# Kernel optimization log

Measured on AMD Instinct MI355X. Metric: run time of the kernel, lower is better.

Reference implementation:

```python
import jax, jax.numpy as jnp
import numpy as np

ENCODER_STRIDE = 320
TEMPERATURE = 1.0


def setup_inputs() -> dict:
    key = jax.random.key(0)
    k1, k2, k3, k4 = jax.random.split(key, 4)
    B, D, T, K = 8, 512, 4096, 4096
    student_features = jax.random.normal(k1, (B, D, T), dtype=jnp.float32)
    codebook = jax.random.normal(k2, (K, D), dtype=jnp.float32)
    teacher_codes = jax.random.randint(k3, (B, T), 0, K, dtype=jnp.int64)
    lengths = jax.random.randint(k4, (B,), 0, T * ENCODER_STRIDE, dtype=jnp.int64)
    return {
        "student_features": student_features,
        "codebook": codebook,
        "teacher_codes": teacher_codes,
        "lengths": lengths,
    }


def reference(student_features, codebook, teacher_codes, lengths):
    B, D, T = student_features.shape
    # length mask over frames: frame t is valid if its start sample < length
    frame_starts = jnp.arange(T, dtype=jnp.int64) * ENCODER_STRIDE  # [T]
    mask = (frame_starts[None, :] < lengths[:, None]).astype(student_features.dtype)  # [B,T]

    z = jnp.transpose(student_features, (0, 2, 1)).reshape(-1, D)  # [N,D], N=B*T

    # cdist p=2: sqrt(|z|^2 + |c|^2 - 2 z.c)
    z2 = jnp.sum(z * z, axis=1, keepdims=True)            # [N,1]
    c2 = jnp.sum(codebook * codebook, axis=1)[None, :]    # [1,K]
    d2 = z2 + c2 - 2.0 * (z @ codebook.T)                 # [N,K]
    dists = jnp.sqrt(jnp.maximum(d2, 1e-12))

    soft_weights = jax.nn.softmax(-dists / TEMPERATURE, axis=1)  # [N,K]
    soft_recon = soft_weights @ codebook                          # [N,D]

    codes_flat = teacher_codes.reshape(-1)                        # [N]
    target_embeddings = jax.lax.stop_gradient(codebook[codes_flat])  # [N,D]

    diff_sq = jnp.mean((soft_recon - target_embeddings) ** 2, axis=1).reshape(B, T)
    loss = jnp.sum(diff_sq * mask) / (jnp.sum(mask) + 1e-8)
    return loss
```

## Files before the change

### kernel.cpp

```cpp
#include <hip/hip_runtime.h>
#include <hip/hip_bf16.h>


#define BB 8
#define DD 512
#define TT 4096
#define KKK 4096
#define ENC_STRIDE 320
#define KT 32
#define NKT (KKK / KT)
#define NW 8
#define ROWS 128
#define KBROW 2056
#define KBBYTES 4112
#define BUFB (8 * KBBYTES)

#define WS_C2    256
#define WS_RTS   16640
#define WS_CBH   32768
#define WS_PART  4227072ULL
#define WS_ML    (WS_PART + 67108864ULL)
#define WS_NEED  (WS_ML + 524288ULL)

typedef __attribute__((ext_vector_type(8))) short bf16x8;
typedef __attribute__((ext_vector_type(4))) float f32x4;

union FragU { bf16x8 v; uint2 h2[2]; ushort us[8]; unsigned long long q[2]; uint4 u4; };

static __device__ __forceinline__ ushort f2bf(float x) {
  unsigned u = __float_as_uint(x);
  unsigned r = (u + 0x7FFFu + ((u >> 16) & 1u)) >> 16;
  return (ushort)r;
}
static __device__ __forceinline__ uint2 f4tobf(float4 v) {
  uint2 r;
  r.x = (unsigned)f2bf(v.x) | ((unsigned)f2bf(v.y) << 16);
  r.y = (unsigned)f2bf(v.z) | ((unsigned)f2bf(v.w) << 16);
  return r;
}
static __device__ __forceinline__ unsigned pk2bf(float lo, float hi) {
  return (__float_as_uint(lo) >> 16) | (__float_as_uint(hi) & 0xFFFF0000u);
}
static __device__ __forceinline__ float bfh2f(ushort h) {
  return __uint_as_float(((unsigned)h) << 16);
}
static __device__ __forceinline__ float fsqrtf(float x) {
  float r; asm("v_sqrt_f32 %0, %1" : "=v"(r) : "v"(x)); return r;
}
static __device__ __forceinline__ void gld_lds16(const void* g, void* l) {
  __builtin_amdgcn_global_load_lds(
      (const __attribute__((address_space(1))) unsigned*)g,
      (__attribute__((address_space(3))) unsigned*)l, 16, 0, 0);
}
static __device__ __forceinline__ unsigned lds_addr(const void* p) {
  return (unsigned)(size_t)(const __attribute__((address_space(3))) char*)p;
}

__global__ __launch_bounds__(256) void vq_prep(const float* __restrict__ cb,
                                               float* __restrict__ c2,
                                               ushort* __restrict__ cbh) {
  int k = blockIdx.x * 4 + (threadIdx.x >> 6);
  int lane = threadIdx.x & 63;
  const float4* p = (const float4*)(cb + (size_t)k * DD + lane * 8);
  float4 a = p[0], b = p[1];
  if (cbh) {
    uint2 pa = f4tobf(a), pb = f4tobf(b);
    *(uint4*)(cbh + (size_t)k * DD + lane * 8) = make_uint4(pa.x, pa.y, pb.x, pb.y);
  }
  float s = a.x*a.x + a.y*a.y + a.z*a.z + a.w*a.w
          + b.x*b.x + b.y*b.y + b.z*b.z + b.w*b.w;
  #pragma unroll
  for (int m = 1; m <= 32; m <<= 1) s += __shfl_xor(s, m);
  if (lane == 0) c2[k] = s;
}

__global__ void vq_plan(const int* __restrict__ lens, int* __restrict__ hdr,
                        int* __restrict__ rts) {
  int n = 0;
  for (int b2 = 0; b2 < BB; ++b2) {
    int v = (lens[b2] + (ENC_STRIDE - 1)) / ENC_STRIDE;
    v = v < TT ? v : TT;
    int tiles = (v + 127) >> 7;
    for (int t = 0; t < tiles; ++t) rts[n++] = (b2 << 5) | t;
  }
  hdr[0] = n;
  hdr[1] = (n * 128 + 255) >> 8;
  hdr[2] = n * 128;
}

__global__ __launch_bounds__(512, 2) void vq_main_ws(
    const float* __restrict__ sf,
    const ushort* __restrict__ cbh,
    const float* __restrict__ c2,
    const int* __restrict__ hdr,
    const int* __restrict__ rts,
    ushort* __restrict__ recon_p,
    float* __restrict__ ml) {
  __shared__ __align__(128) ushort cs[4][8][KBROW];
  __shared__ __align__(16) ushort wlds[2][NW][16][40];
  __shared__ float  alds[2][ROWS];
  __shared__ float  llds[ROWS];
  __shared__ int    flagv[128];

  const int Q = hdr[1], total = hdr[2];
  int start = blockIdx.x * Q;
  if (Q == 0 || start >= total) return;
  int end = start + Q;
  end = end < total ? end : total;
  int slot = blockIdx.x * 2;

  const int tid = threadIdx.x;
  const int w  = tid >> 6;
  const int l  = tid & 63;
  const int lg = l >> 4;
  const int ln = l & 15;
  const int sbase = (w * 4 + ((l >> 1) & 3)) * DD + (l >> 3) * 16 + (l & 1) * 8;
  const unsigned score_lane = (unsigned)((ln >> 2) * KBBYTES + (ln & 3) * 32
                                         + (lg >> 1) * 128 + (lg & 1) * 16);
  const unsigned tr_lane = (unsigned)(lg * KBBYTES + w * 512 + ln * 8);
  const unsigned cs0a = lds_addr(&cs[0][0][0]);

  while (start < end) {
    const int rt = start >> 7;
    const int k0 = start & 127;
    int seg_end = (rt + 1) << 7;
    seg_end = seg_end < end ? seg_end : end;
    const int klen = seg_end - start;
    const int rtv = rts[rt];
    const int b  = rtv >> 5;
    const int t0 = (rtv & 31) << 7;

    for (int i2 = tid; i2 < klen; i2 += 512) flagv[i2] = 0;

    const float* sfb = sf + (size_t)b * DD * TT;
    const int trow = t0 + w * 16 + ln;
    bf16x8 za[16];
    float z2 = 0.f;
    #pragma unroll
    for (int f = 0; f < 16; ++f) {
      #pragma unroll
      for (int j = 0; j < 8; ++j) {
        int d = f * 32 + lg * 8 + j;
        float v = __builtin_nontemporal_load(&sfb[(size_t)d * TT + trow]);
        z2 += v * v;
        za[f][j] = (short)f2bf(v);
      }
    }
    z2 += __shfl_xor(z2, 16);
    z2 += __shfl_xor(z2, 32);

    auto stage = [&](int kta, int buf) {
      const ushort* gb = cbh + (size_t)kta * KT * DD + sbase;
      ushort* lb = &cs[buf][w][0];
      #pragma unroll
      for (int q = 0; q < 4; ++q) gld_lds16(gb + q * 128, lb + q * 512);
    };

    stage(k0, 0);
    if (klen > 1) stage(k0 + 1, 1);
    if (klen > 2) stage(k0 + 2, 2);

    float mrow = -1e30f, lrow = 0.f;
    f32x4 acc[8][4];
    #pragma unroll
    for (int r = 0; r < 8; ++r)
      #pragma unroll
      for (int nt = 0; nt < 4; ++nt) acc[r][nt] = (f32x4){0.f, 0.f, 0.f, 0.f};

    f32x4 sc0, sc1;
    auto scores = [&](int sbuf) {
      const char* csb = (const char*)&cs[sbuf][0][0];
      f32x4 e0s = (f32x4){0,0,0,0}, o0s = (f32x4){0,0,0,0};
      f32x4 e1s = (f32x4){0,0,0,0}, o1s = (f32x4){0,0,0,0};
      __builtin_amdgcn_s_setprio(1);
      #pragma unroll
      for (int f = 0; f < 8; ++f) {
        bf16x8 ae0 = *(const bf16x8*)(csb + score_lane + (2 * f) * 256);
        bf16x8 ao0 = *(const bf16x8*)(csb + score_lane + (2 * f + 1) * 256);
        bf16x8 ae1 = *(const bf16x8*)(csb + score_lane + 16448 + (2 * f) * 256);
        bf16x8 ao1 = *(const bf16x8*)(csb + score_lane + 16448 + (2 * f + 1) * 256);
        e0s = __builtin_amdgcn_mfma_f32_16x16x32_bf16(ae0, za[2 * f],     e0s, 0, 0, 0);
        o0s = __builtin_amdgcn_mfma_f32_16x16x32_bf16(ao0, za[2 * f + 1], o0s, 0, 0, 0);
        e1s = __builtin_amdgcn_mfma_f32_16x16x32_bf16(ae1, za[2 * f],     e1s, 0, 0, 0);
        o1s = __builtin_amdgcn_mfma_f32_16x16x32_bf16(ao1, za[2 * f + 1], o1s, 0, 0, 0);
      }
      __builtin_amdgcn_s_setprio(0);
      sc0 = e0s + o0s;
      sc1 = e1s + o1s;
    };

    auto softmax_full = [&](int kta, int li) {
      const float4 c2a = *(const float4*)(c2 + kta * KT + lg * 4);
      const float4 c2b = *(const float4*)(c2 + kta * KT + 16 + lg * 4);
      float c2v[8] = {c2a.x, c2a.y, c2a.z, c2a.w, c2b.x, c2b.y, c2b.z, c2b.w};
      float sv[8];
      #pragma unroll
      for (int v = 0; v < 4; ++v) {
        sv[v]     = -fsqrtf(fmaxf(z2 + c2v[v]     - 2.f * sc0[v], 1e-12f));
        sv[4 + v] = -fsqrtf(fmaxf(z2 + c2v[4 + v] - 2.f * sc1[v], 1e-12f));
      }
      float lmax = sv[0];
      #pragma unroll
      for (int i = 1; i < 8; ++i) lmax = fmaxf(lmax, sv[i]);
      float tmax = fmaxf(lmax, __shfl_xor(lmax, 16));
      tmax = fmaxf(tmax, __shfl_xor(tmax, 32));
      float el[8], lsum = 0.f;
      #pragma unroll
      for (int i = 0; i < 8; ++i) { el[i] = __expf(sv[i] - lmax); lsum += el[i]; }
      const bool defer = (li > 0) && (tmax <= mrow + 8.f);
      const float mnew = defer ? mrow : fmaxf(tmax, mrow);
      const float factor = __expf(lmax - mnew);
      float esum = lsum * factor;
      esum += __shfl_xor(esum, 16);
      esum += __shfl_xor(esum, 32);
      const float alpha = (li > 0 && !defer) ? __expf(mrow - mnew) : 1.f;
      lrow = lrow * alpha + esum;
      mrow = mnew;
      uint4 pk;
      pk.x = pk2bf(el[0] * factor, el[1] * factor);
      pk.y = pk2bf(el[2] * factor, el[3] * factor);
      pk.z = pk2bf(el[4] * factor, el[5] * factor);
      pk.w = pk2bf(el[6] * factor, el[7] * factor);
      *(uint4*)&wlds[li & 1][w][ln][lg * 8] = pk;
      if (lg == 0) alds[li & 1][w * 16 + ln] = alpha;
      if (li > 0 && !__all(defer) && l == 0) flagv[li] = 1;
    };

    auto recon_full = [&](int lim1) {
      const int s = lim1 & 1;
      const unsigned trb = cs0a + (unsigned)(lim1 & 3) * BUFB + tr_lane;
      unsigned long long tq0[4], tq1[4];
      #pragma unroll
      for (int nt = 0; nt < 4; ++nt) {
        asm volatile("ds_read_b64_tr_b16 %0, %2 offset:%3\n\t"
                     "ds_read_b64_tr_b16 %1, %2 offset:%4"
                     : "=&v"(tq0[nt]), "=&v"(tq1[nt])
                     : "v"(trb), "i"(nt * 128), "i"(16448 + nt * 128));
      }
      const int flg = flagv[lim1];
      asm volatile("s_waitcnt lgkmcnt(0)" ::: "memory");
      __builtin_amdgcn_sched_barrier(0);
      if (flg) {
        #pragma unroll
        for (int r = 0; r < 8; ++r)
          #pragma unroll
          for (int v = 0; v < 4; ++v) {
            float av = alds[s][r * 16 + lg * 4 + v];
            #pragma unroll
            for (int nt = 0; nt < 4; ++nt) acc[r][nt][v] *= av;
          }
      }
      FragU cf[4];
      #pragma unroll
      for (int nt = 0; nt < 4; ++nt) { cf[nt].q[0] = tq0[nt]; cf[nt].q[1] = tq1[nt]; }
      __builtin_amdgcn_s_setprio(1);
      #pragma unroll
      for (int rh = 0; rh < 2; ++rh) {
        bf16x8 wa4[4];
        #pragma unroll
        for (int r4 = 0; r4 < 4; ++r4)
          wa4[r4] = *(const bf16x8*)&wlds[s][rh * 4 + r4][ln][lg * 8];
        #pragma unroll
        for (int r4 = 0; r4 < 4; ++r4)
          #pragma unroll
          for (int nt = 0; nt < 4; ++nt)
            acc[rh * 4 + r4][nt] = __builtin_amdgcn_mfma_f32_16x16x32_bf16(
                wa4[r4], cf[nt].v, acc[rh * 4 + r4][nt], 0, 0, 0);
      }
      __builtin_amdgcn_s_setprio(0);
    };

    __syncthreads();
    scores(0);
    softmax_full(k0, 0);

    if (w < 4) {
      #pragma unroll 1
      for (int li = 1; li < klen; ++li) {
        __syncthreads();
        if (li + 2 < klen) stage(k0 + li + 2, (li + 2) & 3);
        scores(li & 3);
        softmax_full(k0 + li, li);
        recon_full(li - 1);
      }
    } else {
      #pragma unroll 1
      for (int li = 1; li < klen; ++li) {
        __syncthreads();
        if (li + 2 < klen) stage(k0 + li + 2, (li + 2) & 3);
        recon_full(li - 1);
        scores(li & 3);
        softmax_full(k0 + li, li);
      }
    }

    __syncthreads();
    recon_full(klen - 1);

    if (lg == 0) {
      llds[w * 16 + ln] = lrow;
      float2 mlv; mlv.x = mrow; mlv.y = lrow;
      *(float2*)&ml[(size_t)(slot * 128 + w * 16 + ln) * 2] = mlv;
    }
    __syncthreads();
    {
      ushort* rp = recon_p + (size_t)slot * (128 * 512);
      #pragma unroll
      for (int r = 0; r < 8; ++r) {
        #pragma unroll
        for (int v = 0; v < 4; ++v) {
          const int row = r * 16 + lg * 4 + v;
          const float lv = llds[row];
          #pragma unroll
          for (int nt = 0; nt < 4; ++nt) {
            const int d = w * 64 + nt * 16 + ln;
            rp[row * 512 + d] = f2bf(acc[r][nt][v] / lv);
          }
        }
      }
    }
    __syncthreads();

    start += klen;
    slot++;
  }
}

__global__ __launch_bounds__(512) void vq_merge(
    const ushort* __restrict__ recon_p, const float* __restrict__ ml,
    const int* __restrict__ hdr, const int* __restrict__ rts,
    const int* __restrict__ lens, const float* __restrict__ cb,
    const int* __restrict__ codes, float* __restrict__ num) {
  __shared__ float red[64];
  const int i = blockIdx.x;
  const int nact = hdr[0];
  if (i >= nact) return;
  const int Q = hdr[1], total = hdr[2];
  const int rtv = rts[i];
  const int b = rtv >> 5;
  const int t0 = (rtv & 31) << 7;
  int vcount = (lens[b] + (ENC_STRIDE - 1)) / ENC_STRIDE;
  vcount = vcount < TT ? vcount : TT;

  const int tid = threadIdx.x;
  const int rl = tid >> 3;
  const int q  = tid & 7;
  const int r  = blockIdx.y * 64 + rl;
  const int flat0 = i << 7, flat1 = flat0 + 128;
  int c_lo = flat0 / Q;
  int c_hi = (flat1 - 1) / Q;
  c_hi = c_hi < 255 ? c_hi : 255;

  float M = -1e30f;
  for (int c = c_lo; c <= c_hi; ++c) {
    const int cs_ = c * Q;
    int ce = cs_ + Q; ce = ce < total ? ce : total;
    if (cs_ >= flat1 || ce <= flat0) continue;
    const int slot = c * 2 + (i - (cs_ >> 7));
    M = fmaxf(M, ml[(size_t)(slot * 128 + r) * 2]);
  }
  float L = 0.f;
  for (int c = c_lo; c <= c_hi; ++c) {
    const int cs_ = c * Q;
    int ce = cs_ + Q; ce = ce < total ? ce : total;
    if (cs_ >= flat1 || ce <= flat0) continue;
    const int slot = c * 2 + (i - (cs_ >> 7));
    const float m_ = ml[(size_t)(slot * 128 + r) * 2];
    const float l_ = ml[(size_t)(slot * 128 + r) * 2 + 1];
    L += l_ * __expf(m_ - M);
  }
  const float invL = 1.f / L;

  const int tc = codes[b * TT + t0 + r];
  const float* targ = cb + (size_t)tc * DD;

  float psum = 0.f;
  #pragma unroll 1
  for (int ch = 0; ch < 8; ++ch) {
    const int d0 = q * 64 + ch * 8;
    float rec[8] = {0.f, 0.f, 0.f, 0.f, 0.f, 0.f, 0.f, 0.f};
    for (int c = c_lo; c <= c_hi; ++c) {
      const int cs_ = c * Q;
      int ce = cs_ + Q; ce = ce < total ? ce : total;
      if (cs_ >= flat1 || ce <= flat0) continue;
      const int slot = c * 2 + (i - (cs_ >> 7));
      const float m_ = ml[(size_t)(slot * 128 + r) * 2];
      const float l_ = ml[(size_t)(slot * 128 + r) * 2 + 1];
      const float wn = l_ * __expf(m_ - M) * invL;
      const ushort* rp = recon_p + (size_t)slot * (128 * 512) + r * 512 + d0;
      FragU u; u.u4 = *(const uint4*)rp;
      #pragma unroll
      for (int j = 0; j < 8; ++j) rec[j] += wn * bfh2f(u.us[j]);
    }
    const float4 tg0 = *(const float4*)(targ + d0);
    const float4 tg1 = *(const float4*)(targ + d0 + 4);
    float tg[8] = {tg0.x, tg0.y, tg0.z, tg0.w, tg1.x, tg1.y, tg1.z, tg1.w};
    #pragma unroll
    for (int j = 0; j < 8; ++j) { float df = rec[j] - tg[j]; psum += df * df; }
  }
  psum += __shfl_xor(psum, 1);
  psum += __shfl_xor(psum, 2);
  psum += __shfl_xor(psum, 4);
  if (q == 0) red[rl] = ((t0 + r) < vcount) ? psum * (1.f / DD) : 0.f;
  __syncthreads();
  if (tid < 64) {
    float val = red[tid];
    val += __shfl_xor(val, 1);
    val += __shfl_xor(val, 2);
    val += __shfl_xor(val, 4);
    val += __shfl_xor(val, 8);
    val += __shfl_xor(val, 16);
    val += __shfl_xor(val, 32);
    if (tid == 0) atomicAdd(num, val);
  }
}

template <int GLD>
__global__ __launch_bounds__(512, 2) void vq_main(
    const float* __restrict__ sf, const float* __restrict__ cb,
    const ushort* __restrict__ cbh, const int* __restrict__ codes,
    const int* __restrict__ lens, const float* __restrict__ c2,
    float* __restrict__ num) {
  __shared__ __align__(128) ushort cs[4][8][KBROW];
  __shared__ __align__(16) ushort wlds[2][NW][16][40];
  __shared__ float  alds[2][ROWS];
  __shared__ float  llds[ROWS];
  __shared__ float  diffred[ROWS];
  __shared__ int    flagv[NKT];

  const int bid = blockIdx.x;
  const int b  = bid >> 5;
  const int t0 = (bid & 31) << 7;
  const int len = lens[b];
  int vcount = (len + (ENC_STRIDE - 1)) / ENC_STRIDE;
  vcount = vcount < TT ? vcount : TT;
  if (t0 >= vcount) return;

  const int tid = threadIdx.x;
  const int w  = tid >> 6;
  const int l  = tid & 63;
  const int lg = l >> 4;
  const int ln = l & 15;

  for (int i = tid; i < ROWS; i += 512) diffred[i] = 0.f;
  for (int i = tid; i < NKT; i += 512) flagv[i] = 0;

  const float* sfb = sf + (size_t)b * DD * TT;
  const int trow = t0 + w * 16 + ln;
  bf16x8 za[16];
  float z2 = 0.f;
  #pragma unroll
  for (int f = 0; f < 16; ++f) {
    #pragma unroll
    for (int j = 0; j < 8; ++j) {
      int d = f * 32 + lg * 8 + j;
      float v = __builtin_nontemporal_load(&sfb[(size_t)d * TT + trow]);
      z2 += v * v;
      za[f][j] = (short)f2bf(v);
    }
  }
  z2 += __shfl_xor(z2, 16);
  z2 += __shfl_xor(z2, 32);

  const int sbase = (w * 4 + ((l >> 1) & 3)) * DD + (l >> 3) * 16 + (l & 1) * 8;
  auto stage = [&](int kt, int buf) {
    if (GLD) {
      const ushort* gb = cbh + (size_t)kt * KT * DD + sbase;
      ushort* lb = &cs[buf][w][0];
      #pragma unroll
      for (int q = 0; q < 4; ++q) gld_lds16(gb + q * 128, lb + q * 512);
    } else {
      const float* gb = cb + (size_t)kt * KT * DD + sbase;
      #pragma unroll
      for (int q = 0; q < 4; ++q) {
        float4 v0 = *(const float4*)(gb + q * 128);
        float4 v1 = *(const float4*)(gb + q * 128 + 4);
        uint2 a0 = f4tobf(v0), a1 = f4tobf(v1);
        *(uint4*)&cs[buf][w][q * 512 + l * 8] = make_uint4(a0.x, a0.y, a1.x, a1.y);
      }
    }
  };

  stage(0, 0); stage(1, 1); stage(2, 2);

  float mrow = -1e30f, lrow = 0.f;
  f32x4 acc[8][4];
  #pragma unroll
  for (int r = 0; r < 8; ++r)
    #pragma unroll
    for (int nt = 0; nt < 4; ++nt) acc[r][nt] = (f32x4){0.f, 0.f, 0.f, 0.f};

  const unsigned score_lane = (unsigned)((ln >> 2) * KBBYTES + (ln & 3) * 32
                                         + (lg >> 1) * 128 + (lg & 1) * 16);
  const unsigned tr_lane = (unsigned)(lg * KBBYTES + w * 512 + ln * 8);
  const unsigned cs0a = lds_addr(&cs[0][0][0]);

  f32x4 sc0, sc1;
  auto scores = [&](int sbuf) {
    const char* csb = (const char*)&cs[sbuf][0][0];
    f32x4 e0s = (f32x4){0,0,0,0}, o0s = (f32x4){0,0,0,0};
    f32x4 e1s = (f32x4){0,0,0,0}, o1s = (f32x4){0,0,0,0};
    __builtin_amdgcn_s_setprio(1);
    #pragma unroll
    for (int f = 0; f < 8; ++f) {
      bf16x8 ae0 = *(const bf16x8*)(csb + score_lane + (2 * f) * 256);
      bf16x8 ao0 = *(const bf16x8*)(csb + score_lane + (2 * f + 1) * 256);
      bf16x8 ae1 = *(const bf16x8*)(csb + score_lane + 16448 + (2 * f) * 256);
      bf16x8 ao1 = *(const bf16x8*)(csb + score_lane + 16448 + (2 * f + 1) * 256);
      e0s = __builtin_amdgcn_mfma_f32_16x16x32_bf16(ae0, za[2 * f],     e0s, 0, 0, 0);
      o0s = __builtin_amdgcn_mfma_f32_16x16x32_bf16(ao0, za[2 * f + 1], o0s, 0, 0, 0);
      e1s = __builtin_amdgcn_mfma_f32_16x16x32_bf16(ae1, za[2 * f],     e1s, 0, 0, 0);
      o1s = __builtin_amdgcn_mfma_f32_16x16x32_bf16(ao1, za[2 * f + 1], o1s, 0, 0, 0);
    }
    __builtin_amdgcn_s_setprio(0);
    sc0 = e0s + o0s;
    sc1 = e1s + o1s;
  };

  auto softmax_full = [&](int kta, int li) {
    const float4 c2a = *(const float4*)(c2 + kta * KT + lg * 4);
    const float4 c2b = *(const float4*)(c2 + kta * KT + 16 + lg * 4);
    float c2v[8] = {c2a.x, c2a.y, c2a.z, c2a.w, c2b.x, c2b.y, c2b.z, c2b.w};
    float sv[8];
    #pragma unroll
    for (int v = 0; v < 4; ++v) {
      sv[v]     = -fsqrtf(fmaxf(z2 + c2v[v]     - 2.f * sc0[v], 1e-12f));
      sv[4 + v] = -fsqrtf(fmaxf(z2 + c2v[4 + v] - 2.f * sc1[v], 1e-12f));
    }
    float lmax = sv[0];
    #pragma unroll
    for (int i = 1; i < 8; ++i) lmax = fmaxf(lmax, sv[i]);
    float tmax = fmaxf(lmax, __shfl_xor(lmax, 16));
    tmax = fmaxf(tmax, __shfl_xor(tmax, 32));
    float el[8], lsum = 0.f;
    #pragma unroll
    for (int i = 0; i < 8; ++i) { el[i] = __expf(sv[i] - lmax); lsum += el[i]; }
    const bool defer = (li > 0) && (tmax <= mrow + 8.f);
    const float mnew = defer ? mrow : fmaxf(tmax, mrow);
    const float factor = __expf(lmax - mnew);
    float esum = lsum * factor;
    esum += __shfl_xor(esum, 16);
    esum += __shfl_xor(esum, 32);
    const float alpha = (li > 0 && !defer) ? __expf(mrow - mnew) : 1.f;
    lrow = lrow * alpha + esum;
    mrow = mnew;
    uint4 pk;
    pk.x = pk2bf(el[0] * factor, el[1] * factor);
    pk.y = pk2bf(el[2] * factor, el[3] * factor);
    pk.z = pk2bf(el[4] * factor, el[5] * factor);
    pk.w = pk2bf(el[6] * factor, el[7] * factor);
    *(uint4*)&wlds[li & 1][w][ln][lg * 8] = pk;
    if (lg == 0) alds[li & 1][w * 16 + ln] = alpha;
    if (li > 0 && !__all(defer) && l == 0) flagv[li] = 1;
  };

  auto recon_full = [&](int lim1) {
    const int s = lim1 & 1;
    const unsigned trb = cs0a + (unsigned)(lim1 & 3) * BUFB + tr_lane;
    unsigned long long tq0[4], tq1[4];
    #pragma unroll
    for (int nt = 0; nt < 4; ++nt) {
      asm volatile("ds_read_b64_tr_b16 %0, %2 offset:%3\n\t"
                   "ds_read_b64_tr_b16 %1, %2 offset:%4"
                   : "=&v"(tq0[nt]), "=&v"(tq1[nt])
                   : "v"(trb), "i"(nt * 128), "i"(16448 + nt * 128));
    }
    const int flg = flagv[lim1];
    asm volatile("s_waitcnt lgkmcnt(0)" ::: "memory");
    __builtin_amdgcn_sched_barrier(0);
    if (flg) {
      #pragma unroll
      for (int r = 0; r < 8; ++r)
        #pragma unroll
        for (int v = 0; v < 4; ++v) {
          float av = alds[s][r * 16 + lg * 4 + v];
          #pragma unroll
          for (int nt = 0; nt < 4; ++nt) acc[r][nt][v] *= av;
        }
    }
    FragU cf[4];
    #pragma unroll
    for (int nt = 0; nt < 4; ++nt) { cf[nt].q[0] = tq0[nt]; cf[nt].q[1] = tq1[nt]; }
    __builtin_amdgcn_s_setprio(1);
    #pragma unroll
    for (int rh = 0; rh < 2; ++rh) {
      bf16x8 wa4[4];
      #pragma unroll
      for (int r4 = 0; r4 < 4; ++r4)
        wa4[r4] = *(const bf16x8*)&wlds[s][rh * 4 + r4][ln][lg * 8];
      #pragma unroll
      for (int r4 = 0; r4 < 4; ++r4)
        #pragma unroll
        for (int nt = 0; nt < 4; ++nt)
          acc[rh * 4 + r4][nt] = __builtin_amdgcn_mfma_f32_16x16x32_bf16(
              wa4[r4], cf[nt].v, acc[rh * 4 + r4][nt], 0, 0, 0);
    }
    __builtin_amdgcn_s_setprio(0);
  };

  __syncthreads();
  scores(0);
  softmax_full(0, 0);

  if (w < 4) {
    #pragma unroll 1
    for (int it = 1; it < NKT; ++it) {
      __syncthreads();
      if (it + 2 < NKT) stage(it + 2, (it + 2) & 3);
      scores(it & 3);
      softmax_full(it, it);
      recon_full(it - 1);
    }
  } else {
    #pragma unroll 1
    for (int it = 1; it < NKT; ++it) {
      __syncthreads();
      if (it + 2 < NKT) stage(it + 2, (it + 2) & 3);
      recon_full(it - 1);
      scores(it & 3);
      softmax_full(it, it);
    }
  }

  __syncthreads();
  recon_full(NKT - 1);

  if (lg == 0) llds[w * 16 + ln] = lrow;
  __syncthreads();
  const int* tcodes = codes + b * TT + t0;
  #pragma unroll
  for (int r = 0; r < 8; ++r) {
    float pv[4];
    #pragma unroll
    for (int v = 0; v < 4; ++v) {
      const int row = r * 16 + lg * 4 + v;
      const float lv = llds[row];
      const int tc = tcodes[row];
      const float* erow = cb + (size_t)tc * DD + w * 64;
      float ps = 0.f;
      #pragma unroll
      for (int nt = 0; nt < 4; ++nt) {
        float rc = acc[r][nt][v] / lv;
        float df = rc - erow[nt * 16 + ln];
        ps += df * df;
      }
      pv[v] = ps;
    }
    #pragma unroll
    for (int v = 0; v < 4; ++v) {
      pv[v] += __shfl_xor(pv[v], 1);
      pv[v] += __shfl_xor(pv[v], 2);
      pv[v] += __shfl_xor(pv[v], 4);
      pv[v] += __shfl_xor(pv[v], 8);
    }
    if (ln == 0) {
      #pragma unroll
      for (int v = 0; v < 4; ++v)
        atomicAdd(&diffred[r * 16 + lg * 4 + v], pv[v]);
    }
  }
  __syncthreads();
  if (tid < ROWS) {
    float val = (t0 + tid < vcount) ? diffred[tid] * (1.f / DD) : 0.f;
    val += __shfl_xor(val, 1);
    val += __shfl_xor(val, 2);
    val += __shfl_xor(val, 4);
    val += __shfl_xor(val, 8);
    val += __shfl_xor(val, 16);
    val += __shfl_xor(val, 32);
    if ((tid & 63) == 0) atomicAdd(num, val);
  }
}

__global__ void vq_finalize(const float* __restrict__ num,
                            const int* __restrict__ lens,
                            float* __restrict__ out) {
  float denom = 0.f;
  for (int b = 0; b < BB; ++b) {
    int v = (lens[b] + (ENC_STRIDE - 1)) / ENC_STRIDE;
    v = v < TT ? v : TT;
    denom += (float)v;
  }
  out[0] = num[0] / (denom + 1e-8f);
}

extern "C" void kernel_launch(void* const* d_in, const int* in_sizes, int n_in,
                              void* d_out, int out_size, void* d_ws, size_t ws_size,
                              hipStream_t stream) {
  const float* sf    = (const float*)d_in[0];
  const float* cb    = (const float*)d_in[1];
  const int*   codes = (const int*)d_in[2];
  const int*   lens  = (const int*)d_in[3];
  float* out = (float*)d_out;
  float* num = (float*)d_ws;
  int*   hdr = (int*)((char*)d_ws + 16);
  float* c2  = (float*)((char*)d_ws + WS_C2);
  int*   rts = (int*)((char*)d_ws + WS_RTS);
  const size_t need_gld = WS_CBH + (size_t)KKK * DD * sizeof(ushort);
  ushort* cbh = (ws_size >= need_gld) ? (ushort*)((char*)d_ws + WS_CBH) : nullptr;

  (void)hipMemsetAsync(d_ws, 0, 4, stream);
  vq_prep<<<KKK / 4, 256, 0, stream>>>(cb, c2, cbh);

  if (cbh && ws_size >= WS_NEED) {
    ushort* recon_p = (ushort*)((char*)d_ws + WS_PART);
    float*  mlp     = (float*)((char*)d_ws + WS_ML);
    vq_plan<<<1, 1, 0, stream>>>(lens, hdr, rts);
    vq_main_ws<<<256, 512, 0, stream>>>(sf, cbh, c2, hdr, rts, recon_p, mlp);
    vq_merge<<<dim3(256, 2), 512, 0, stream>>>(recon_p, mlp, hdr, rts, lens, cb, codes, num);
  } else {
    const int grid = (BB * TT) / ROWS;
    if (cbh)
      vq_main<1><<<grid, 512, 0, stream>>>(sf, cb, cbh, codes, lens, c2, num);
    else
      vq_main<0><<<grid, 512, 0, stream>>>(sf, cb, cbh, codes, lens, c2, num);
  }
  vq_finalize<<<1, 1, 0, stream>>>(num, lens, out);
}
```

Before: 375.7 us.

## Fold tile planning into prep kernel and read score operands from global for half the waves

After: 575.8 us. 53.3% more time.

```diff
diff --git a/kernel.cpp b/kernel.cpp
--- a/kernel.cpp
+++ b/kernel.cpp
@@ -58,7 +58,22 @@
 
 __global__ __launch_bounds__(256) void vq_prep(const float* __restrict__ cb,
                                                float* __restrict__ c2,
-                                               ushort* __restrict__ cbh) {
+                                               ushort* __restrict__ cbh,
+                                               const int* __restrict__ lens,
+                                               int* __restrict__ hdr,
+                                               int* __restrict__ rts) {
+  if (blockIdx.x == 0 && threadIdx.x == 0 && hdr) {
+    int n = 0;
+    for (int b2 = 0; b2 < BB; ++b2) {
+      int v = (lens[b2] + (ENC_STRIDE - 1)) / ENC_STRIDE;
+      v = v < TT ? v : TT;
+      int tiles = (v + 127) >> 7;
+      for (int t = 0; t < tiles; ++t) rts[n++] = (b2 << 5) | t;
+    }
+    hdr[0] = n;
+    hdr[1] = (n * 128 + 255) >> 8;
+    hdr[2] = n * 128;
+  }
   int k = blockIdx.x * 4 + (threadIdx.x >> 6);
   int lane = threadIdx.x & 63;
   const float4* p = (const float4*)(cb + (size_t)k * DD + lane * 8);
@@ -72,20 +87,6 @@
   #pragma unroll
   for (int m = 1; m <= 32; m <<= 1) s += __shfl_xor(s, m);
   if (lane == 0) c2[k] = s;
-}
-
-__global__ void vq_plan(const int* __restrict__ lens, int* __restrict__ hdr,
-                        int* __restrict__ rts) {
-  int n = 0;
-  for (int b2 = 0; b2 < BB; ++b2) {
-    int v = (lens[b2] + (ENC_STRIDE - 1)) / ENC_STRIDE;
-    v = v < TT ? v : TT;
-    int tiles = (v + 127) >> 7;
-    for (int t = 0; t < tiles; ++t) rts[n++] = (b2 << 5) | t;
-  }
-  hdr[0] = n;
-  hdr[1] = (n * 128 + 255) >> 8;
-  hdr[2] = n * 128;
 }
 
 __global__ __launch_bounds__(512, 2) void vq_main_ws(
@@ -119,6 +120,8 @@
                                          + (lg >> 1) * 128 + (lg & 1) * 16);
   const unsigned tr_lane = (unsigned)(lg * KBBYTES + w * 512 + ln * 8);
   const unsigned cs0a = lds_addr(&cs[0][0][0]);
+  const ushort* gsc0 = cbh + (size_t)ln * DD + lg * 8;
+  const ushort* gsc1 = cbh + (size_t)(16 + ln) * DD + lg * 8;
 
   while (start < end) {
     const int rt = start >> 7;
@@ -168,23 +171,42 @@
       for (int nt = 0; nt < 4; ++nt) acc[r][nt] = (f32x4){0.f, 0.f, 0.f, 0.f};
 
     f32x4 sc0, sc1;
-    auto scores = [&](int sbuf) {
-      const char* csb = (const char*)&cs[sbuf][0][0];
+    auto scores = [&](int kta, int sbuf) {
       f32x4 e0s = (f32x4){0,0,0,0}, o0s = (f32x4){0,0,0,0};
       f32x4 e1s = (f32x4){0,0,0,0}, o1s = (f32x4){0,0,0,0};
-      __builtin_amdgcn_s_setprio(1);
-      #pragma unroll
-      for (int f = 0; f < 8; ++f) {
-        bf16x8 ae0 = *(const bf16x8*)(csb + score_lane + (2 * f) * 256);
-        bf16x8 ao0 = *(const bf16x8*)(csb + score_lane + (2 * f + 1) * 256);
-        bf16x8 ae1 = *(const bf16x8*)(csb + score_lane + 16448 + (2 * f) * 256);
-        bf16x8 ao1 = *(const bf16x8*)(csb + score_lane + 16448 + (2 * f + 1) * 256);
-        e0s = __builtin_amdgcn_mfma_f32_16x16x32_bf16(ae0, za[2 * f],     e0s, 0, 0, 0);
-        o0s = __builtin_amdgcn_mfma_f32_16x16x32_bf16(ao0, za[2 * f + 1], o0s, 0, 0, 0);
-        e1s = __builtin_amdgcn_mfma_f32_16x16x32_bf16(ae1, za[2 * f],     e1s, 0, 0, 0);
-        o1s = __builtin_amdgcn_mfma_f32_16x16x32_bf16(ao1, za[2 * f + 1], o1s, 0, 0, 0);
-      }
-      __builtin_amdgcn_s_setprio(0);
+      if (w < 4) {
+        const char* csb = (const char*)&cs[sbuf][0][0];
+        __builtin_amdgcn_s_setprio(1);
+        #pragma unroll
+        for (int f = 0; f < 8; ++f) {
+          bf16x8 ae0 = *(const bf16x8*)(csb + score_lane + (2 * f) * 256);
+          bf16x8 ao0 = *(const bf16x8*)(csb + score_lane + (2 * f + 1) * 256);
+          bf16x8 ae1 = *(const bf16x8*)(csb + score_lane + 16448 + (2 * f) * 256);
+          bf16x8 ao1 = *(const bf16x8*)(csb + score_lane + 16448 + (2 * f + 1) * 256);
+          e0s = __builtin_amdgcn_mfma_f32_16x16x32_bf16(ae0, za[2 * f],     e0s, 0, 0, 0);
+          o0s = __builtin_amdgcn_mfma_f32_16x16x32_bf16(ao0, za[2 * f + 1], o0s, 0, 0, 0);
+          e1s = __builtin_amdgcn_mfma_f32_16x16x32_bf16(ae1, za[2 * f],     e1s, 0, 0, 0);
+          o1s = __builtin_amdgcn_mfma_f32_16x16x32_bf16(ao1, za[2 * f + 1], o1s, 0, 0, 0);
+        }
+        __builtin_amdgcn_s_setprio(0);
+      } else {
+        const size_t goff = (size_t)kta * KT * DD;
+        const ushort* g0 = gsc0 + goff;
+        const ushort* g1 = gsc1 + goff;
+        __builtin_amdgcn_s_setprio(1);
+        #pragma unroll
+        for (int f = 0; f < 8; ++f) {
+          bf16x8 ae0 = *(const bf16x8*)(g0 + (2 * f) * 32);
+          bf16x8 ao0 = *(const bf16x8*)(g0 + (2 * f + 1) * 32);
+          bf16x8 ae1 = *(const bf16x8*)(g1 + (2 * f) * 32);
+          bf16x8 ao1 = *(const bf16x8*)(g1 + (2 * f + 1) * 32);
+          e0s = __builtin_amdgcn_mfma_f32_16x16x32_bf16(ae0, za[2 * f],     e0s, 0, 0, 0);
+          o0s = __builtin_amdgcn_mfma_f32_16x16x32_bf16(ao0, za[2 * f + 1], o0s, 0, 0, 0);
+          e1s = __builtin_amdgcn_mfma_f32_16x16x32_bf16(ae1, za[2 * f],     e1s, 0, 0, 0);
+          o1s = __builtin_amdgcn_mfma_f32_16x16x32_bf16(ao1, za[2 * f + 1], o1s, 0, 0, 0);
+        }
+        __builtin_amdgcn_s_setprio(0);
+      }
       sc0 = e0s + o0s;
       sc1 = e1s + o1s;
     };
@@ -271,7 +293,7 @@
     };
 
     __syncthreads();
-    scores(0);
+    scores(k0, 0);
     softmax_full(k0, 0);
 
     if (w < 4) {
@@ -279,7 +301,7 @@
       for (int li = 1; li < klen; ++li) {
         __syncthreads();
         if (li + 2 < klen) stage(k0 + li + 2, (li + 2) & 3);
-        scores(li & 3);
+        scores(k0 + li, li & 3);
         softmax_full(k0 + li, li);
         recon_full(li - 1);
       }
@@ -289,7 +311,7 @@
         __syncthreads();
         if (li + 2 < klen) stage(k0 + li + 2, (li + 2) & 3);
         recon_full(li - 1);
-        scores(li & 3);
+        scores(k0 + li, li & 3);
         softmax_full(k0 + li, li);
       }
     }
@@ -698,14 +720,15 @@
   int*   rts = (int*)((char*)d_ws + WS_RTS);
   const size_t need_gld = WS_CBH + (size_t)KKK * DD * sizeof(ushort);
   ushort* cbh = (ws_size >= need_gld) ? (ushort*)((char*)d_ws + WS_CBH) : nullptr;
+  const bool ws_path = (cbh != nullptr) && (ws_size >= WS_NEED);
 
   (void)hipMemsetAsync(d_ws, 0, 4, stream);
-  vq_prep<<<KKK / 4, 256, 0, stream>>>(cb, c2, cbh);
-
-  if (cbh && ws_size >= WS_NEED) {
+  vq_prep<<<KKK / 4, 256, 0, stream>>>(cb, c2, cbh, lens,
+                                       ws_path ? hdr : nullptr, rts);
+
+  if (ws_path) {
     ushort* recon_p = (ushort*)((char*)d_ws + WS_PART);
     float*  mlp     = (float*)((char*)d_ws + WS_ML);
-    vq_plan<<<1, 1, 0, stream>>>(lens, hdr, rts);
     vq_main_ws<<<256, 512, 0, stream>>>(sf, cbh, c2, hdr, rts, recon_p, mlp);
     vq_merge<<<dim3(256, 2), 512, 0, stream>>>(recon_p, mlp, hdr, rts, lens, cb, codes, num);
   } else {
```
